# Kernel tuning notes

Measured on AMD Instinct MI355X. Metric: run time of the kernel, lower is better.

## Reference

```python
import jax, jax.numpy as jnp
import numpy as np

DIM = 64   # voxel grid resolution per axis
C = 64     # channels (C_in == num_outputs, required by residual add)
N = 200000 # number of points
EPS = 1e-3 # keras BatchNormalization default epsilon

def _bn(x, g, b, m, v):
    # inference-mode batch norm
    return (x - m) * jax.lax.rsqrt(v + EPS) * g + b

def _conv3d_relu(x, k, b):
    # x: [1,X,Y,Z,Cin], k: [3,3,3,Cin,Cout] (DHWIO), 'same' padding, relu activation
    y = jax.lax.conv_general_dilated(x, k, (1, 1, 1), 'SAME',
        dimension_numbers=('NDHWC', 'DHWIO', 'NDHWC'))
    return jax.nn.relu(y + b)

def _trilinear(grid, pts):
    # grid: [X,Y,Z,C], pts: [N,3] in voxel coordinates
    dmax = jnp.asarray(grid.shape[:3], pts.dtype) - 1.0
    p = jnp.clip(pts, 0.0, dmax)
    f = jnp.floor(p)
    t = p - f  # [N,3] fractional part
    i0 = f.astype(jnp.int32)
    i1 = jnp.minimum(i0 + 1, jnp.asarray(grid.shape[:3], jnp.int32) - 1)
    out = jnp.zeros((pts.shape[0], grid.shape[-1]), grid.dtype)
    for dx in (0, 1):
        for dy in (0, 1):
            for dz in (0, 1):
                ix = i1[:, 0] if dx else i0[:, 0]
                iy = i1[:, 1] if dy else i0[:, 1]
                iz = i1[:, 2] if dz else i0[:, 2]
                w = ((t[:, 0] if dx else 1.0 - t[:, 0])
                     * (t[:, 1] if dy else 1.0 - t[:, 1])
                     * (t[:, 2] if dz else 1.0 - t[:, 2]))
                out = out + w[:, None] * grid[ix, iy, iz]
    return out

def setup_inputs():
    key = jax.random.key(0)
    ks = jax.random.split(key, 10)
    inputs = jax.random.normal(ks[0], (N, C), jnp.float32)
    # pt_coords already scaled into voxel space (VOXEL_SIZE_INV folded in)
    pt_coords = jax.random.uniform(ks[1], (N, 3), jnp.float32) * (DIM - 1)
    voxel_indexes = jax.random.randint(ks[2], (N, 3), 0, DIM)
    pts_per_voxel_inv = jax.random.uniform(ks[3], (1, DIM, DIM, DIM, 1), jnp.float32)
    s = 1.0 / np.sqrt(C)
    w_mlp = jax.random.normal(ks[4], (C, C), jnp.float32) * s
    b_mlp = jnp.zeros((C,), jnp.float32)
    sk = 1.0 / np.sqrt(27 * C)
    k1 = jax.random.normal(ks[5], (3, 3, 3, C, C), jnp.float32) * sk
    cb1 = jnp.zeros((C,), jnp.float32)
    k2 = jax.random.normal(ks[6], (3, 3, 3, C, C), jnp.float32) * sk
    cb2 = jnp.zeros((C,), jnp.float32)
    def bn_params(k):
        a, b_, c = jax.random.split(k, 3)
        g = 1.0 + 0.1 * jax.random.normal(a, (C,), jnp.float32)
        be = 0.1 * jax.random.normal(b_, (C,), jnp.float32)
        m = 0.1 * jax.random.normal(c, (C,), jnp.float32)
        v = jnp.ones((C,), jnp.float32)
        return g, be, m, v
    g0, be0, m0, v0 = bn_params(ks[7])
    g1, be1, m1, v1 = bn_params(ks[8])
    g2, be2, m2, v2 = bn_params(ks[9])
    return dict(inputs=inputs, pt_coords=pt_coords, voxel_indexes=voxel_indexes,
                pts_per_voxel_inv=pts_per_voxel_inv, w_mlp=w_mlp, b_mlp=b_mlp,
                g0=g0, be0=be0, m0=m0, v0=v0, k1=k1, cb1=cb1, g1=g1, be1=be1,
                m1=m1, v1=v1, k2=k2, cb2=cb2, g2=g2, be2=be2, m2=m2, v2=v2)

def reference(inputs, pt_coords, voxel_indexes, pts_per_voxel_inv, w_mlp, b_mlp,
              g0, be0, m0, v0, k1, cb1, g1, be1, m1, v1, k2, cb2, g2, be2, m2, v2):
    # point branch: Dense(relu) + BN
    mlp_out = _bn(jax.nn.relu(inputs @ w_mlp + b_mlp), g0, be0, m0, v0)
    # voxelize: scatter_nd adds duplicate-index contributions
    voxels = jnp.zeros((DIM, DIM, DIM, C), inputs.dtype).at[
        voxel_indexes[:, 0], voxel_indexes[:, 1], voxel_indexes[:, 2]].add(inputs)
    voxels = voxels[None] * pts_per_voxel_inv  # per-voxel mean normalization
    # voxel branch: two Conv3D(relu)+BN
    h = _bn(_conv3d_relu(voxels, k1, cb1), g1, be1, m1, v1)
    h = _bn(_conv3d_relu(h, k2, cb2), g2, be2, m2, v2)
    # devoxelize: trilinear gather back to points (coords already in voxel space)
    vox_out = _trilinear(h[0], pt_coords)
    return mlp_out + vox_out
```

## Files before the change

### kernel.cpp

```cpp
#include <hip/hip_runtime.h>
#include <hip/hip_bf16.h>

#define DIMV 64
#define CH 64
#define EPSB 1e-3f

using bf16x8 = __attribute__((ext_vector_type(8))) short;
using f32x16 = __attribute__((ext_vector_type(16))) float;

__device__ __forceinline__ unsigned short f2bf(float f) {
    union { float f; unsigned u; } x; x.f = f;
    unsigned r = x.u + 0x7fff + ((x.u >> 16) & 1);
    return (unsigned short)(r >> 16);
}
__device__ __forceinline__ float bf2f(unsigned short u) {
    union { unsigned u; float f; } x; x.u = ((unsigned)u) << 16;
    return x.f;
}

__global__ void scatter_kernel(const float* __restrict__ x, const int* __restrict__ idx,
                               float* __restrict__ grid, int n_total) {
    int tid = blockIdx.x * blockDim.x + threadIdx.x;
    if (tid >= n_total) return;
    int n = tid >> 6, c = tid & 63;
    int ix = idx[n * 3 + 0], iy = idx[n * 3 + 1], iz = idx[n * 3 + 2];
    atomicAdd(&grid[(size_t)(((ix * DIMV) + iy) * DIMV + iz) * CH + c], x[tid]);
}

__global__ void pack_kernel(const float* __restrict__ A, const float* __restrict__ inv,
                            unsigned short* __restrict__ G1) {
    int t = blockIdx.x * 256 + threadIdx.x;
    if (t >= (DIMV * DIMV * DIMV * CH) / 8) return;
    int v = t >> 3, c8 = (t & 7) * 8;
    const float* src = A + (size_t)v * CH + c8;
    float s = inv[v];
    __align__(16) unsigned short tmp[8];
#pragma unroll
    for (int j = 0; j < 8; ++j) tmp[j] = f2bf(src[j] * s);
    *(int4*)(G1 + (size_t)t * 8) = *(const int4*)tmp;
}

__global__ void wprep_all(const float* __restrict__ K1, const float* __restrict__ K2,
                          const float* __restrict__ Wm, unsigned short* __restrict__ wbuf1,
                          unsigned short* __restrict__ wbuf2, unsigned short* __restrict__ wm) {
    int t = blockIdx.x * 256 + threadIdx.x;
    if (t >= 2 * 110592 + 4096) return;
    const float* src;
    unsigned short* dst;
    int tt;
    if (t < 110592) { src = K1; dst = wbuf1; tt = t; }
    else if (t < 221184) { src = K2; dst = wbuf2; tt = t - 110592; }
    else { src = Wm; dst = wm; tt = t - 221184; }
    int j = tt & 7;
    int l = (tt >> 3) & 63;
    int nt = (tt >> 9) & 1;
    int kkl = (tt >> 10) & 3;
    int d = tt >> 12;
    int ci = kkl * 16 + (l >> 5) * 8 + j;
    int co = nt * 32 + (l & 31);
    dst[tt] = f2bf(src[((size_t)d * 64 + ci) * 64 + co]);
}

__global__ __launch_bounds__(512) void conv_mfma(
    const unsigned short* __restrict__ G, const unsigned short* __restrict__ wbuf,
    const float* __restrict__ cb, const float* __restrict__ g,
    const float* __restrict__ be, const float* __restrict__ m,
    const float* __restrict__ v, unsigned short* __restrict__ out) {
    __shared__ __align__(16) unsigned short slab[272 * 128];
    const int tid = threadIdx.x;
    const int lane = tid & 63;
    const int w = tid >> 6;
    const int cx = (w >> 2) & 1;
    const int cy = (w >> 1) & 1;
    const int ntw = w & 1;
    const int lz = lane & 31;
    const int kg = lane >> 5;
    const int BX = blockIdx.x, BY = blockIdx.y, BZ = blockIdx.z;
    const int x0 = 2 * BX - 1, y0 = 2 * BY - 1;
    const int zbase = 32 * BZ - 1;

#pragma unroll
    for (int it = 0; it < 9; ++it) {
        int idx = it * 512 + tid;
        if (idx < 4352) {
            int s = idx & 15;
            int r = idx >> 4;
            int zp = r % 17;
            int rxy = r / 17;
            int xx = x0 + (rxy >> 2);
            int yy = y0 + (rxy & 3);
            int cp = s ^ (zp & 15);
            int c = cp >> 1, p = cp & 1;
            int zz = zbase + 2 * zp + p;
            int4 val = make_int4(0, 0, 0, 0);
            if ((unsigned)xx < DIMV && (unsigned)yy < DIMV && (unsigned)zz < DIMV)
                val = *(const int4*)(G + (size_t)(((xx * DIMV) + yy) * DIMV + zz) * CH + c * 8);
            *(int4*)(slab + (size_t)idx * 8) = val;
        }
    }
    __syncthreads();

    f32x16 acc;
#pragma unroll
    for (int r = 0; r < 16; ++r) acc[r] = 0.f;

    bf16x8 bfr0[4], bfr1[4];
#pragma unroll
    for (int q = 0; q < 4; ++q)
        bfr0[q] = *(const bf16x8*)(wbuf + q * 1024 + ntw * 512 + lane * 8);

#pragma unroll
    for (int d = 0; d < 27; ++d) {
        if (d < 26) {
            const unsigned short* wn = wbuf + (size_t)(d + 1) * 4096 + ntw * 512 + lane * 8;
            if (d & 1) {
#pragma unroll
                for (int q = 0; q < 4; ++q) bfr0[q] = *(const bf16x8*)(wn + q * 1024);
            } else {
#pragma unroll
                for (int q = 0; q < 4; ++q) bfr1[q] = *(const bf16x8*)(wn + q * 1024);
            }
        }
        const int dx = d / 9, dy = (d / 3) % 3, dz = d % 3;
        const int zval = lz + dz;
        const int zp = zval >> 1, p = zval & 1;
        const int rbase = ((cx + dx) * 4 + (cy + dy)) * 17 + zp;
#pragma unroll
        for (int kkl = 0; kkl < 4; ++kkl) {
            const int c = kkl * 2 + kg;
            const int slot = (c * 2 + p) ^ (zp & 15);
            bf16x8 a = *(const bf16x8*)(slab + rbase * 128 + slot * 8);
            bf16x8 b = (d & 1) ? bfr1[kkl] : bfr0[kkl];
            acc = __builtin_amdgcn_mfma_f32_32x32x16_bf16(a, b, acc, 0, 0, 0);
        }
    }

    const int x_out = 2 * BX + cx;
    const int y_out = 2 * BY + cy;
    const int co = ntw * 32 + lz;
    float scale = g[co] * rsqrtf(v[co] + EPSB);
    float shift = be[co] - m[co] * scale;
    float bias = cb[co];
    size_t base = (size_t)((x_out * DIMV) + y_out) * DIMV * CH + co;
#pragma unroll
    for (int r = 0; r < 16; ++r) {
        int zrow = (r & 3) + 8 * (r >> 2) + 4 * kg;
        int z = BZ * 32 + zrow;
        float val = fmaxf(acc[r] + bias, 0.f) * scale + shift;
        out[base + (size_t)z * CH] = f2bf(val);
    }
}

__global__ __launch_bounds__(256) void mlp_gather(
    const float* __restrict__ x, const unsigned short* __restrict__ wfrag,
    const float* __restrict__ b, const float* __restrict__ g,
    const float* __restrict__ be, const float* __restrict__ m,
    const float* __restrict__ v, const unsigned short* __restrict__ grid,
    const float* __restrict__ pts, float* __restrict__ out, int npts) {
    __shared__ float lds[128 * 64];
    const int w = threadIdx.x >> 6;
    const int lane = threadIdx.x & 63;
    const int col = lane & 31;
    const int kg = lane >> 5;
    const int p0 = (blockIdx.x * 4 + w) * 32;

    if (p0 < npts) {
        bf16x8 a[4];
        const float* xr = x + (size_t)(p0 + col) * CH + kg * 8;
#pragma unroll
        for (int kk = 0; kk < 4; ++kk) {
            const float* p = xr + kk * 16;
            bf16x8 t;
#pragma unroll
            for (int j = 0; j < 8; ++j) t[j] = (short)f2bf(p[j]);
            a[kk] = t;
        }
        f32x16 acc[2];
#pragma unroll
        for (int nt = 0; nt < 2; ++nt)
#pragma unroll
            for (int r = 0; r < 16; ++r) acc[nt][r] = 0.f;
#pragma unroll
        for (int kk = 0; kk < 4; ++kk) {
            bf16x8 b0 = *(const bf16x8*)(wfrag + (kk * 2 + 0) * 512 + lane * 8);
            bf16x8 b1 = *(const bf16x8*)(wfrag + (kk * 2 + 1) * 512 + lane * 8);
            acc[0] = __builtin_amdgcn_mfma_f32_32x32x16_bf16(a[kk], b0, acc[0], 0, 0, 0);
            acc[1] = __builtin_amdgcn_mfma_f32_32x32x16_bf16(a[kk], b1, acc[1], 0, 0, 0);
        }
#pragma unroll
        for (int nt = 0; nt < 2; ++nt) {
            int co = nt * 32 + col;
            float scale = g[co] * rsqrtf(v[co] + EPSB);
            float shift = be[co] - m[co] * scale;
            float bias = b[co];
#pragma unroll
            for (int r = 0; r < 16; ++r) {
                int row = (r & 3) + 8 * (r >> 2) + 4 * kg;
                float val = fmaxf(acc[nt][r] + bias, 0.f) * scale + shift;
                lds[(w * 32 + row) * 64 + co] = val;
            }
        }
    }
    __syncthreads();

    const int pblk = blockIdx.x * 128;
#pragma unroll 4
    for (int i = 0; i < 32; ++i) {
        int idx = i * 256 + threadIdx.x;
        int pl = idx >> 6;
        int c = idx & 63;
        int pt = pblk + pl;
        if (pt >= npts) break;
        float px = fminf(fmaxf(pts[pt * 3 + 0], 0.f), (float)(DIMV - 1));
        float py = fminf(fmaxf(pts[pt * 3 + 1], 0.f), (float)(DIMV - 1));
        float pz = fminf(fmaxf(pts[pt * 3 + 2], 0.f), (float)(DIMV - 1));
        float fx = floorf(px), fy = floorf(py), fz = floorf(pz);
        float tx = px - fx, ty = py - fy, tz = pz - fz;
        int x0 = (int)fx, y0 = (int)fy, z0 = (int)fz;
        int x1 = min(x0 + 1, DIMV - 1), y1 = min(y0 + 1, DIMV - 1), z1 = min(z0 + 1, DIMV - 1);
        float wx0 = 1.f - tx, wy0 = 1.f - ty, wz0 = 1.f - tz;
        float acc = lds[pl * 64 + c];
        acc = fmaf(wx0 * wy0 * wz0, bf2f(grid[(size_t)(((x0 * DIMV) + y0) * DIMV + z0) * CH + c]), acc);
        acc = fmaf(wx0 * wy0 * tz,  bf2f(grid[(size_t)(((x0 * DIMV) + y0) * DIMV + z1) * CH + c]), acc);
        acc = fmaf(wx0 * ty * wz0,  bf2f(grid[(size_t)(((x0 * DIMV) + y1) * DIMV + z0) * CH + c]), acc);
        acc = fmaf(wx0 * ty * tz,   bf2f(grid[(size_t)(((x0 * DIMV) + y1) * DIMV + z1) * CH + c]), acc);
        acc = fmaf(tx * wy0 * wz0,  bf2f(grid[(size_t)(((x1 * DIMV) + y0) * DIMV + z0) * CH + c]), acc);
        acc = fmaf(tx * wy0 * tz,   bf2f(grid[(size_t)(((x1 * DIMV) + y0) * DIMV + z1) * CH + c]), acc);
        acc = fmaf(tx * ty * wz0,   bf2f(grid[(size_t)(((x1 * DIMV) + y1) * DIMV + z0) * CH + c]), acc);
        acc = fmaf(tx * ty * tz,    bf2f(grid[(size_t)(((x1 * DIMV) + y1) * DIMV + z1) * CH + c]), acc);
        out[(size_t)pt * CH + c] = acc;
    }
}

extern "C" void kernel_launch(void* const* d_in, const int* in_sizes, int n_in,
                              void* d_out, int out_size, void* d_ws, size_t ws_size,
                              hipStream_t stream) {
    const float* inputs = (const float*)d_in[0];
    const float* pt_coords = (const float*)d_in[1];
    const int* voxel_indexes = (const int*)d_in[2];
    const float* ppvi = (const float*)d_in[3];
    const float* w_mlp = (const float*)d_in[4];
    const float* b_mlp = (const float*)d_in[5];
    const float* g0 = (const float*)d_in[6];
    const float* be0 = (const float*)d_in[7];
    const float* m0 = (const float*)d_in[8];
    const float* v0 = (const float*)d_in[9];
    const float* k1 = (const float*)d_in[10];
    const float* cb1 = (const float*)d_in[11];
    const float* g1 = (const float*)d_in[12];
    const float* be1 = (const float*)d_in[13];
    const float* m1 = (const float*)d_in[14];
    const float* v1 = (const float*)d_in[15];
    const float* k2 = (const float*)d_in[16];
    const float* cb2 = (const float*)d_in[17];
    const float* g2 = (const float*)d_in[18];
    const float* be2 = (const float*)d_in[19];
    const float* m2 = (const float*)d_in[20];
    const float* v2 = (const float*)d_in[21];
    float* out = (float*)d_out;

    char* ws = (char*)d_ws;
    float* A = (float*)ws;
    unsigned short* G2 = (unsigned short*)ws;
    unsigned short* G3 = (unsigned short*)(ws + 33554432);
    unsigned short* G1 = (unsigned short*)(ws + 67108864);
    unsigned short* wbuf1 = (unsigned short*)(ws + 100663296);
    unsigned short* wbuf2 = (unsigned short*)(ws + 100884480);
    unsigned short* wmlp = (unsigned short*)(ws + 101105664);

    const int n_total = in_sizes[0];
    const int npts = n_total / CH;
    const int nblk = (n_total + 255) / 256;
    const size_t grid_elems = (size_t)DIMV * DIMV * DIMV * CH;

    hipMemsetAsync(A, 0, grid_elems * sizeof(float), stream);
    wprep_all<<<880, 256, 0, stream>>>(k1, k2, w_mlp, wbuf1, wbuf2, wmlp);
    scatter_kernel<<<nblk, 256, 0, stream>>>(inputs, voxel_indexes, A, n_total);
    pack_kernel<<<(int)(grid_elems / 8 + 255) / 256, 256, 0, stream>>>(A, ppvi, G1);

    dim3 cgrid(32, 32, 2);
    conv_mfma<<<cgrid, 512, 0, stream>>>(G1, wbuf1, cb1, g1, be1, m1, v1, G2);
    conv_mfma<<<cgrid, 512, 0, stream>>>(G2, wbuf2, cb2, g2, be2, m2, v2, G3);

    mlp_gather<<<(npts + 127) / 128, 256, 0, stream>>>(
        inputs, wmlp, b_mlp, g0, be0, m0, v0, G3, pt_coords, out, npts);
}
```

Baseline: 296.0 us.

## Scatter directly into bf16 grid with packed bf16 atomics, dropping fp32 pack pass

Points are scaled by the per-voxel inverse count before scattering and then accumulated straight into the bf16 conv input grid with global_atomic_pk_add_bf16, two channels per atomic. This removes the 64MB fp32 accumulation buffer, its memset, and the separate pack kernel that re-read it and converted it to bf16. The cost is that duplicate-index sums now accumulate in bf16 precision, which adds rounding error, and the build depends on inline asm for the packed bf16 atomic.

```diff
diff --git a/kernel.cpp b/kernel.cpp
--- a/kernel.cpp
+++ b/kernel.cpp
@@ -18,26 +18,20 @@
     return x.f;
 }
 
-__global__ void scatter_kernel(const float* __restrict__ x, const int* __restrict__ idx,
-                               float* __restrict__ grid, int n_total) {
+__global__ void scatter_bf16(const float* __restrict__ x, const int* __restrict__ idx,
+                             const float* __restrict__ inv, unsigned short* __restrict__ grid,
+                             int n2) {
     int tid = blockIdx.x * blockDim.x + threadIdx.x;
-    if (tid >= n_total) return;
-    int n = tid >> 6, c = tid & 63;
+    if (tid >= n2) return;
+    int n = tid >> 5, c2 = tid & 31;
     int ix = idx[n * 3 + 0], iy = idx[n * 3 + 1], iz = idx[n * 3 + 2];
-    atomicAdd(&grid[(size_t)(((ix * DIMV) + iy) * DIMV + iz) * CH + c], x[tid]);
-}
-
-__global__ void pack_kernel(const float* __restrict__ A, const float* __restrict__ inv,
-                            unsigned short* __restrict__ G1) {
-    int t = blockIdx.x * 256 + threadIdx.x;
-    if (t >= (DIMV * DIMV * DIMV * CH) / 8) return;
-    int v = t >> 3, c8 = (t & 7) * 8;
-    const float* src = A + (size_t)v * CH + c8;
-    float s = inv[v];
-    __align__(16) unsigned short tmp[8];
-#pragma unroll
-    for (int j = 0; j < 8; ++j) tmp[j] = f2bf(src[j] * s);
-    *(int4*)(G1 + (size_t)t * 8) = *(const int4*)tmp;
+    int vox = ((ix * DIMV) + iy) * DIMV + iz;
+    float s = inv[vox];
+    float v0 = x[(size_t)n * CH + c2 * 2 + 0] * s;
+    float v1 = x[(size_t)n * CH + c2 * 2 + 1] * s;
+    unsigned pk = (unsigned)f2bf(v0) | ((unsigned)f2bf(v1) << 16);
+    unsigned short* addr = grid + (size_t)vox * CH + c2 * 2;
+    asm volatile("global_atomic_pk_add_bf16 %0, %1, off" :: "v"(addr), "v"(pk) : "memory");
 }
 
 __global__ void wprep_all(const float* __restrict__ K1, const float* __restrict__ K2,
@@ -260,7 +254,6 @@
     float* out = (float*)d_out;
 
     char* ws = (char*)d_ws;
-    float* A = (float*)ws;
     unsigned short* G2 = (unsigned short*)ws;
     unsigned short* G3 = (unsigned short*)(ws + 33554432);
     unsigned short* G1 = (unsigned short*)(ws + 67108864);
@@ -270,13 +263,12 @@
 
     const int n_total = in_sizes[0];
     const int npts = n_total / CH;
-    const int nblk = (n_total + 255) / 256;
+    const int n2 = npts * 32;
     const size_t grid_elems = (size_t)DIMV * DIMV * DIMV * CH;
 
-    hipMemsetAsync(A, 0, grid_elems * sizeof(float), stream);
+    hipMemsetAsync(G1, 0, grid_elems * sizeof(unsigned short), stream);
     wprep_all<<<880, 256, 0, stream>>>(k1, k2, w_mlp, wbuf1, wbuf2, wmlp);
-    scatter_kernel<<<nblk, 256, 0, stream>>>(inputs, voxel_indexes, A, n_total);
-    pack_kernel<<<(int)(grid_elems / 8 + 255) / 256, 256, 0, stream>>>(A, ppvi, G1);
+    scatter_bf16<<<(n2 + 255) / 256, 256, 0, stream>>>(inputs, voxel_indexes, ppvi, G1, n2);
 
     dim3 cgrid(32, 32, 2);
     conv_mfma<<<cgrid, 512, 0, stream>>>(G1, wbuf1, cb1, g1, be1, m1, v1, G2);
```

Result: faster. 253.3 us, median of 3 (-14.4%).
